# Optimization experiments

Hardware: AMD Instinct MI355X
Metric: run time of the kernel (lower is better)

## Reference

```python
import jax, jax.numpy as jnp
import numpy as np

NEG = -1e30  # log-space 'zero'


def setup_inputs() -> dict:
    N, T, IDIM, V, S = 16, 1024, 512, 4096, 128
    key = jax.random.key(0)
    k0, k1, k2, k3, k4 = jax.random.split(key, 5)
    hs = jax.random.normal(k0, (N, T, IDIM), dtype=jnp.float32)
    hlens = jax.random.randint(k1, (N,), T // 2, T + 1).astype(jnp.int32)
    ys = jax.random.randint(k2, (N, S), 1, V).astype(jnp.int32)  # labels exclude blank=0
    ylens = jax.random.randint(k3, (N,), S // 2, S + 1).astype(jnp.int32)
    W = jax.random.normal(k4, (V, IDIM), dtype=jnp.float32) * 0.02
    b = jnp.zeros((V,), dtype=jnp.float32)
    return {"hs": hs, "hlens": hlens, "ys": ys, "ylens": ylens, "W": W, "b": b}


def _ctc_loss(logp, hlens, ys, ylens):
    # logp: (N, T, V) log-softmax outputs; blank index = 0
    N, T, V = logp.shape
    S = ys.shape[1]
    L = 2 * S + 1
    # extended label sequence: blank, y1, blank, y2, ..., blank
    ext = jnp.zeros((N, L), dtype=ys.dtype).at[:, 1::2].set(ys)  # (N, L)
    s_idx = jnp.arange(L)
    ext_prev2 = jnp.pad(ext, ((0, 0), (2, 0)))[:, :L]
    allow_skip = (ext != 0) & (ext != ext_prev2) & (s_idx[None, :] >= 2)  # (N, L)
    Ln = 2 * ylens + 1  # valid extended length per sample

    lpT = jnp.swapaxes(logp, 0, 1)  # (T, N, V)

    # t = 0 init
    alpha0 = jnp.full((N, L), NEG, dtype=logp.dtype)
    alpha0 = alpha0.at[:, 0].set(lpT[0, :, 0])
    alpha0 = alpha0.at[:, 1].set(jnp.take_along_axis(lpT[0], ys[:, :1], axis=1)[:, 0])

    def step(alpha, xs):
        lp_t, t = xs  # lp_t: (N, V)
        lp_ext = jnp.take_along_axis(lp_t, ext, axis=1)  # (N, L)
        a1 = alpha
        a2 = jnp.pad(alpha, ((0, 0), (1, 0)), constant_values=NEG)[:, :L]
        a3 = jnp.pad(alpha, ((0, 0), (2, 0)), constant_values=NEG)[:, :L]
        a3 = jnp.where(allow_skip, a3, NEG)
        new = jnp.logaddexp(jnp.logaddexp(a1, a2), a3) + lp_ext
        new = jnp.where(s_idx[None, :] < Ln[:, None], new, NEG)
        alpha = jnp.where((t < hlens)[:, None], new, alpha)
        return alpha, None

    ts = jnp.arange(1, T, dtype=hlens.dtype)
    alpha, _ = jax.lax.scan(step, alpha0, (lpT[1:], ts))

    end1 = jnp.take_along_axis(alpha, (Ln - 1)[:, None], axis=1)[:, 0]
    end2 = jnp.take_along_axis(alpha, (Ln - 2)[:, None], axis=1)[:, 0]
    ll = jnp.logaddexp(end1, end2)  # (N,)
    per = jnp.where(ll > -1e29, -ll, 0.0)  # zero_infinity=True
    return jnp.sum(per) / N  # reduction='sum' then divided by len(hlens)


def reference(hs, hlens, ys, ylens, W, b):
    logits = jnp.einsum('nti,vi->ntv', hs, W) + b  # (N, T, V)
    logp = jax.nn.log_softmax(logits, axis=-1)
    return _ctc_loss(logp, hlens, ys, ylens)
```

## Files before the change

kernel.cpp:

```cpp
#include <hip/hip_runtime.h>
#include <cstdint>
#include <cstddef>

using short8_t = __attribute__((ext_vector_type(8))) short;
using f32x4    = __attribute__((ext_vector_type(4))) float;
typedef unsigned short bfu16;

constexpr int   Nn   = 16;
constexpr int   Tt   = 1024;
constexpr int   IDIM = 512;
constexpr int   Vv   = 4096;
constexpr int   Ss   = 128;
constexpr int   Ll   = 2 * Ss + 1;
constexpr int   LS   = 132;
constexpr float NEGV = -1e30f;
constexpr float L2E  = 1.4426950408889634f;
constexpr float LN2  = 0.6931471805599453f;

__device__ __forceinline__ float fexp2(float x) { return __builtin_amdgcn_exp2f(x); }
__device__ __forceinline__ float flog2(float x) { return __builtin_amdgcn_logf(x); }

__device__ __forceinline__ bfu16 f2bf(float f) {
  unsigned int x = __float_as_uint(f);
  x = x + 0x7fffu + ((x >> 16) & 1u);
  return (bfu16)(x >> 16);
}

__device__ __forceinline__ void async16(const void* g, void* l) {
  __builtin_amdgcn_global_load_lds(
      (__attribute__((address_space(1))) void*)(g),
      (__attribute__((address_space(3))) void*)(l), 16, 0, 0);
}

__global__ void convert_zero(const float4* __restrict__ hs4,
                             const float4* __restrict__ W4,
                             ushort4* __restrict__ hsb4,
                             ushort4* __restrict__ Wb4,
                             float* __restrict__ out) {
  if (blockIdx.x == 0 && threadIdx.x == 0) out[0] = 0.f;
  const int HS4 = (Nn * Tt * IDIM) / 4;
  const int TOT = HS4 + (Vv * IDIM) / 4;
  for (int i = blockIdx.x * 256 + threadIdx.x; i < TOT; i += gridDim.x * 256) {
    float4 f;
    if (i < HS4) f = hs4[i]; else f = W4[i - HS4];
    ushort4 o;
    o.x = f2bf(f.x); o.y = f2bf(f.y); o.z = f2bf(f.z); o.w = f2bf(f.w);
    if (i < HS4) hsb4[i] = o; else Wb4[i - HS4] = o;
  }
}

__global__ void build_labels(const int* __restrict__ ys,
                             int* __restrict__ labmap,
                             int* __restrict__ extidx,
                             int* __restrict__ skipflag) {
  const int n = blockIdx.x, tid = threadIdx.x;
  int* lm = labmap + n * Vv;
  for (int v = tid; v < Vv; v += 256) lm[v] = 0x7fffffff;
  __syncthreads();
  if (tid == 0) lm[0] = 0;
  if (tid < Ss) atomicMin(&lm[ys[n * Ss + tid]], tid + 1);
  __syncthreads();
  for (int s = tid; s < Ll; s += 256) {
    int v = (s & 1) ? ys[n * Ss + ((s - 1) >> 1)] : 0;
    extidx[n * Ll + s] = lm[v];
    int allow = 0;
    if ((s & 1) && s >= 3) allow = (v != ys[n * Ss + ((s - 3) >> 1)]) ? 1 : 0;
    skipflag[n * Ll + s] = allow;
  }
  __syncthreads();
  for (int v = tid; v < Vv; v += 256)
    if (lm[v] == 0x7fffffff) lm[v] = -1;
}

__global__ __launch_bounds__(512, 2) void gemm_lse(
    const bfu16* __restrict__ A,
    const bfu16* __restrict__ B,
    const float* __restrict__ bias,
    const int*   __restrict__ labmap,
    float* __restrict__ plab,
    float* __restrict__ psum) {
  __shared__ alignas(128) char ldsraw[131072];
  const int tid  = threadIdx.x;
  const int lane = tid & 63, wid = tid >> 6;
  const int wr = wid >> 2, wc = wid & 3;

  const int flat = blockIdx.x;
  const int wg   = (flat & 7) * 128 + (flat >> 3);
  const int bR = wg >> 4, bC = wg & 15;
  const int rowbase = bR * 256, colbase = bC * 256;

  f32x4 acc[8][4];
#pragma unroll
  for (int m = 0; m < 8; m++)
#pragma unroll
    for (int n = 0; n < 4; n++) {
      f32x4 z = {0.f, 0.f, 0.f, 0.f};
      acc[m][n] = z;
    }

  const int  sw  = wid & 3;
  const bool isB = wid >= 4;
  const char* gsrc0 = (const char*)(isB ? (const void*)B : (const void*)A)
      + (size_t)((isB ? colbase : rowbase) + sw * 64 + (lane >> 3)) * (IDIM * 2)
      + (((lane & 7) ^ ((lane >> 3) & 7)) * 16);
  char* ldst0 = ldsraw + (isB ? 32768 : 0) + sw * 8192;

  const int fr = lane & 15;
  const int g  = lane >> 4;
  const int fx = fr & 7;

  const int nsamp = bR >> 2;
  const int* lm = labmap + nsamp * Vv;
  float bc[4];
  int   slot[4];
#pragma unroll
  for (int n = 0; n < 4; n++) {
    int c = colbase + wc * 64 + n * 16 + fr;
    bc[n]   = bias[c];
    slot[n] = lm[c];
  }

  auto stage = [&](int b, int t) {
#pragma unroll
    for (int i = 0; i < 8; ++i)
      async16(gsrc0 + (size_t)t * 128 + i * 8192, ldst0 + b * 65536 + i * 1024);
  };

  stage(0, 0);
  asm volatile("s_waitcnt vmcnt(0)" ::: "memory");
  __builtin_amdgcn_s_barrier();

  int buf = 0;
  for (int t = 0; t < 8; ++t) {
    const char* Ab = ldsraw + buf * 65536;
    const char* Bb = Ab + 32768;
    if (t < 7) stage(buf ^ 1, t + 1);

    short8_t a0[4], a1[4], a2[4], a3[4], b0[4], b1[4];
#pragma unroll
    for (int m = 0; m < 4; m++)
      a0[m] = *(const short8_t*)(Ab + (wr * 128 + m * 16 + fr) * 128 + ((0 + g) ^ fx) * 16);
#pragma unroll
    for (int n = 0; n < 4; n++)
      b0[n] = *(const short8_t*)(Bb + (wc * 64 + n * 16 + fr) * 128 + ((0 + g) ^ fx) * 16);
#pragma unroll
    for (int m = 0; m < 4; m++)
      a1[m] = *(const short8_t*)(Ab + (wr * 128 + (m + 4) * 16 + fr) * 128 + ((0 + g) ^ fx) * 16);

    __builtin_amdgcn_s_setprio(1);
#pragma unroll
    for (int m = 0; m < 4; m++)
#pragma unroll
      for (int n = 0; n < 4; n++)
        acc[m][n] = __builtin_amdgcn_mfma_f32_16x16x32_bf16(a0[m], b0[n], acc[m][n], 0, 0, 0);
    __builtin_amdgcn_s_setprio(0);

#pragma unroll
    for (int m = 0; m < 4; m++)
      a2[m] = *(const short8_t*)(Ab + (wr * 128 + m * 16 + fr) * 128 + ((4 + g) ^ fx) * 16);
#pragma unroll
    for (int n = 0; n < 4; n++)
      b1[n] = *(const short8_t*)(Bb + (wc * 64 + n * 16 + fr) * 128 + ((4 + g) ^ fx) * 16);

    __builtin_amdgcn_s_setprio(1);
#pragma unroll
    for (int m = 0; m < 4; m++)
#pragma unroll
      for (int n = 0; n < 4; n++)
        acc[m + 4][n] = __builtin_amdgcn_mfma_f32_16x16x32_bf16(a1[m], b0[n], acc[m + 4][n], 0, 0, 0);
    __builtin_amdgcn_s_setprio(0);

#pragma unroll
    for (int m = 0; m < 4; m++)
      a3[m] = *(const short8_t*)(Ab + (wr * 128 + (m + 4) * 16 + fr) * 128 + ((4 + g) ^ fx) * 16);

    __builtin_amdgcn_s_setprio(1);
#pragma unroll
    for (int m = 0; m < 4; m++)
#pragma unroll
      for (int n = 0; n < 4; n++)
        acc[m][n] = __builtin_amdgcn_mfma_f32_16x16x32_bf16(a2[m], b1[n], acc[m][n], 0, 0, 0);
    __builtin_amdgcn_s_setprio(0);

    __builtin_amdgcn_s_setprio(1);
#pragma unroll
    for (int m = 0; m < 4; m++)
#pragma unroll
      for (int n = 0; n < 4; n++)
        acc[m + 4][n] = __builtin_amdgcn_mfma_f32_16x16x32_bf16(a3[m], b1[n], acc[m + 4][n], 0, 0, 0);
    __builtin_amdgcn_s_setprio(0);

    asm volatile("s_waitcnt vmcnt(0)" ::: "memory");
    __builtin_amdgcn_s_barrier();
    buf ^= 1;
  }

  const int g4 = g * 4;
#pragma unroll
  for (int m = 0; m < 8; m++) {
#pragma unroll
    for (int r = 0; r < 4; r++) {
      int row = rowbase + wr * 128 + m * 16 + g4 + r;
      float e0 = fexp2((acc[m][0][r] + bc[0]) * L2E);
      float e1 = fexp2((acc[m][1][r] + bc[1]) * L2E);
      float e2 = fexp2((acc[m][2][r] + bc[2]) * L2E);
      float e3 = fexp2((acc[m][3][r] + bc[3]) * L2E);
      if (slot[0] >= 0) plab[(size_t)row * LS + slot[0]] = e0;
      if (slot[1] >= 0) plab[(size_t)row * LS + slot[1]] = e1;
      if (slot[2] >= 0) plab[(size_t)row * LS + slot[2]] = e2;
      if (slot[3] >= 0) plab[(size_t)row * LS + slot[3]] = e3;
      float s = (e0 + e1) + (e2 + e3);
      s += __shfl_xor(s, 1);
      s += __shfl_xor(s, 2);
      s += __shfl_xor(s, 4);
      s += __shfl_xor(s, 8);
      if (fr == 0) {
        int pc = bC * 4 + wc;
        psum[(size_t)pc * 16384 + row] = s;
      }
    }
  }
}

__global__ void lse_reduce(const float* __restrict__ psum,
                           float* __restrict__ lse) {
  int row = blockIdx.x * 256 + threadIdx.x;
  float s = 0.f;
#pragma unroll 8
  for (int j = 0; j < 64; j++)
    s += psum[(size_t)j * 16384 + row];
  lse[row] = flog2(s) * LN2;
}

constexpr int BRK = 16;

__global__ __launch_bounds__(64) void ctc_dp(
    const float* __restrict__ plab, const float* __restrict__ lse,
    const int* __restrict__ extidx, const int* __restrict__ skipflag,
    const int* __restrict__ hlens, const int* __restrict__ ylens,
    float* __restrict__ out) {
  __shared__ float lbuf[2][2304];
  __shared__ float alf[264];
  const int n    = blockIdx.x;
  const int lane = threadIdx.x;
  const int hlen = hlens[n];
  const int Ln   = 2 * ylens[n] + 1;
  const int sbase = lane * 4;

  const int   e1  = extidx[n * Ll + sbase + 1];
  const int   e3  = extidx[n * Ll + sbase + 3];
  const float sk1 = skipflag[n * Ll + sbase + 1] ? 1.f : 0.f;
  const float sk3 = skipflag[n * Ll + sbase + 3] ? 1.f : 0.f;
  const float skh = (lane > 0 && skipflag[n * Ll + sbase - 1]) ? 1.f : 0.f;
  const float skz = (lane > 0 && skipflag[n * Ll + sbase - 3]) ? 1.f : 0.f;
  const float skv = (lane > 1 && skipflag[n * Ll + sbase - 5]) ? 1.f : 0.f;
  const bool  l0  = (lane == 0);
  const bool  l01 = (lane < 2);
  const float m0  = (sbase + 0 < Ln) ? 1.f : 0.f;
  const float m1  = (sbase + 1 < Ln) ? 1.f : 0.f;
  const float m2  = (sbase + 2 < Ln) ? 1.f : 0.f;
  const float m3  = (sbase + 3 < Ln) ? 1.f : 0.f;
  const float m4  = (lane == 63 && Ln == 257) ? 1.f : 0.f;

  const float* pl  = plab + (size_t)n * Tt * LS;
  const float* lsp = lse + n * Tt;

  float slse = 0.f;
#pragma unroll
  for (int j = 0; j < 16; j++) {
    int t = lane + 64 * j;
    float v = lsp[t];
    slse += (t < hlen) ? v : 0.f;
  }
#pragma unroll
  for (int off = 32; off; off >>= 1) slse += __shfl_xor(slse, off);

  float a0 = 0.f, a1 = 0.f, a2 = 0.f, a3 = 0.f, a4 = 0.f;
  if (l0) { a0 = pl[0]; a1 = pl[e1]; }

  int sc = 0;

  auto pair2 = [&](float pbA, float p1A, float p3A,
                   float pbB, float p1B, float p3B) {
    float pa3 = __shfl_up(a3, 1);
    float pa2 = __shfl_up(a2, 1);
    float pa1 = __shfl_up(a1, 1);
    float prA = __shfl_up(p3A, 1);
    pa3 = l0 ? 0.f : pa3;
    pa2 = l0 ? 0.f : pa2;
    pa1 = l0 ? 0.f : pa1;
    float h1 = (pa3 + pa2 + skh * pa1) * prA;
    float s4 = (a4 + a3) * pbA;
    float s3 = (a3 + a2 + sk3 * a1) * p3A;
    float s2 = (a2 + a1) * pbA;
    float s1 = (a1 + a0 + sk1 * pa3) * p1A;
    float s0 = (a0 + pa3) * pbA;
    a4 = (s4 + s3) * pbB;
    a3 = (s3 + s2 + sk3 * s1) * p3B;
    a2 = (s2 + s1) * pbB;
    a1 = (s1 + s0 + sk1 * h1) * p1B;
    a0 = (s0 + h1) * pbB;
  };

  auto step1 = [&](float pb, float p1, float p3) {
    float pm1 = __shfl_up(a3, 1);
    pm1 = l0 ? 0.f : pm1;
    float n4 = (a4 + a3) * pb;
    float n3 = (a3 + a2 + sk3 * a1) * p3;
    float n2 = (a2 + a1) * pb;
    float n1 = (a1 + a0 + sk1 * pm1) * p1;
    float n0 = (a0 + pm1) * pb;
    a0 = n0; a1 = n1; a2 = n2; a3 = n3; a4 = n4;
  };

  auto rescale = [&]() {
    a0 *= m0; a1 *= m1; a2 *= m2; a3 *= m3; a4 *= m4;
    float mx = fmaxf(fmaxf(a0, a1), fmaxf(a2, a3));
    mx = fmaxf(mx, a4);
#pragma unroll
    for (int off = 32; off; off >>= 1) mx = fmaxf(mx, __shfl_xor(mx, off));
    int ee = (int)((__float_as_uint(mx) >> 23) & 0xff) - 127;
    ee = (mx > 0.f) ? ee : 0;
    float s = __uint_as_float((unsigned)(127 - ee) << 23);
    sc += ee;
    a0 *= s; a1 *= s; a2 *= s; a3 *= s; a4 *= s;
  };

  auto stageblk = [&](int bsel, int row0) {
    const char* src = (const char*)(pl + (size_t)row0 * LS);
    char* dst = (char*)&lbuf[bsel][0];
#pragma unroll
    for (int i = 0; i < 9; ++i)
      async16(src + i * 1024 + lane * 16, dst + i * 1024);
  };

  float rpb[2][4], rp1[2][4], rp3[2][4];
  float rx3[2][3];
  float rz1[2][2];
  float rv3[2][1];

  auto loadring = [&](int slot, const float* Lb, int q) {
#pragma unroll
    for (int r = 0; r < 4; r++) {
      const float* base = Lb + (4 * q + r) * 132;
      rpb[slot][r] = base[0];
      rp1[slot][r] = base[e1];
      rp3[slot][r] = base[e3];
    }
#pragma unroll
    for (int r = 0; r < 3; r++) rx3[slot][r] = __shfl_up(rp3[slot][r], 1);
#pragma unroll
    for (int r = 0; r < 2; r++) rz1[slot][r] = __shfl_up(rp1[slot][r], 1);
    rv3[slot][0] = __shfl_up(rp3[slot][0], 2);
  };

  auto quad4 = [&](int slot) {
    float x0 = __shfl_up(a3, 1);
    float y0 = __shfl_up(a2, 1);
    float z0 = __shfl_up(a1, 1);
    float w0 = __shfl_up(a0, 1);
    float v0 = __shfl_up(a3, 2);
    float u0 = __shfl_up(a2, 2);
    float q0 = __shfl_up(a1, 2);
    x0 = l0 ? 0.f : x0;  y0 = l0 ? 0.f : y0;
    z0 = l0 ? 0.f : z0;  w0 = l0 ? 0.f : w0;
    v0 = l01 ? 0.f : v0; u0 = l01 ? 0.f : u0; q0 = l01 ? 0.f : q0;

    float v1 = (v0 + u0 + skv * q0) * rv3[slot][0];
    float w1 = (w0 + v0) * rpb[slot][0];
    float z1 = (z0 + w0 + skz * v0) * rz1[slot][0];
    float y1 = (y0 + z0) * rpb[slot][0];
    float x1 = (x0 + y0 + skh * z0) * rx3[slot][0];
    float z2 = (z1 + w1 + skz * v1) * rz1[slot][1];
    float y2 = (y1 + z1) * rpb[slot][1];
    float x2 = (x1 + y1 + skh * z1) * rx3[slot][1];
    float x3 = (x2 + y2 + skh * z2) * rx3[slot][2];

    float xk[4] = {x0, x1, x2, x3};
#pragma unroll
    for (int r = 0; r < 4; r++) {
      float pb = rpb[slot][r], p1 = rp1[slot][r], p3 = rp3[slot][r];
      float n4 = (a4 + a3) * pb;
      float n3 = (a3 + a2 + sk3 * a1) * p3;
      float n2 = (a2 + a1) * pb;
      float n1 = (a1 + a0 + sk1 * xk[r]) * p1;
      float n0 = (a0 + xk[r]) * pb;
      a0 = n0; a1 = n1; a2 = n2; a3 = n3; a4 = n4;
    }
  };

  const int nsteps = hlen - 1;
  const int nblk   = nsteps / BRK;

  if (nblk > 0) {
    stageblk(0, 1);
    asm volatile("s_waitcnt vmcnt(0)" ::: "memory");
  }

  for (int b = 0; b < nblk; b++) {
    if (b + 1 < nblk) stageblk((b + 1) & 1, 1 + BRK * (b + 1));
    const float* Lb = &lbuf[b & 1][0];
    loadring(0, Lb, 0);
#pragma unroll
    for (int q = 0; q < 4; q++) {
      if (q < 3) loadring((q + 1) & 1, Lb, q + 1);
      quad4(q & 1);
    }
    if ((b & 1) || b == nblk - 1) rescale();
    asm volatile("s_waitcnt vmcnt(0)" ::: "memory");
  }

  int t = 1 + nblk * BRK;
  for (; t + 1 <= nsteps; t += 2) {
    pair2(pl[(size_t)t * LS], pl[(size_t)t * LS + e1], pl[(size_t)t * LS + e3],
          pl[(size_t)(t + 1) * LS], pl[(size_t)(t + 1) * LS + e1], pl[(size_t)(t + 1) * LS + e3]);
  }
  if (t <= nsteps) {
    step1(pl[(size_t)t * LS], pl[(size_t)t * LS + e1], pl[(size_t)t * LS + e3]);
  }
  rescale();

  alf[sbase + 0] = a0; alf[sbase + 1] = a1;
  alf[sbase + 2] = a2; alf[sbase + 3] = a3;
  if (lane == 63) alf[256] = a4;
  __syncthreads();
  if (l0) {
    float sum = alf[Ln - 1] + alf[Ln - 2];
    float per = 0.f;
    if (sum > 0.f) {
      float llv = (flog2(sum) + (float)sc) * LN2 - slse;
      if (llv > -1e29f) per = -llv;
    }
    atomicAdd(out, per * (1.0f / 16.0f));
  }
}

extern "C" void kernel_launch(void* const* d_in, const int* in_sizes, int n_in,
                              void* d_out, int out_size, void* d_ws, size_t ws_size,
                              hipStream_t stream) {
  const float* hs    = (const float*)d_in[0];
  const int*   hlens = (const int*)d_in[1];
  const int*   ys    = (const int*)d_in[2];
  const int*   ylens = (const int*)d_in[3];
  const float* W     = (const float*)d_in[4];
  const float* bias  = (const float*)d_in[5];
  float*       out   = (float*)d_out;
  char*        ws    = (char*)d_ws;

  const size_t off_hsb    = 0;
  const size_t off_Wb     = off_hsb    + (size_t)Nn*Tt*IDIM*2;
  const size_t off_plab   = off_Wb     + (size_t)Vv*IDIM*2;
  const size_t off_psum   = off_plab   + (size_t)Nn*Tt*LS*4;
  const size_t off_lse    = off_psum   + (size_t)64*16384*4;
  const size_t off_labmap = off_lse    + (size_t)16384*4;
  const size_t off_extidx = off_labmap + (size_t)Nn*Vv*4;
  const size_t off_skip   = off_extidx + (size_t)((Nn*Ll*4 + 255) & ~255);

  bfu16* hsb    = (bfu16*)(ws + off_hsb);
  bfu16* Wb     = (bfu16*)(ws + off_Wb);
  float* plab   = (float*)(ws + off_plab);
  float* psum   = (float*)(ws + off_psum);
  float* lse    = (float*)(ws + off_lse);
  int*   labmap = (int*)(ws + off_labmap);
  int*   extidx = (int*)(ws + off_extidx);
  int*   skipf  = (int*)(ws + off_skip);

  convert_zero<<<2048, 256, 0, stream>>>(
      (const float4*)hs, (const float4*)W, (ushort4*)hsb, (ushort4*)Wb, out);
  build_labels<<<16, 256, 0, stream>>>(ys, labmap, extidx, skipf);
  gemm_lse<<<1024, 512, 0, stream>>>(hsb, Wb, bias, labmap, plab, psum);
  lse_reduce<<<64, 256, 0, stream>>>(psum, lse);
  ctc_dp<<<16, 64, 0, stream>>>(plab, lse, extidx, skipf, hlens, ylens, out);
}
```

Before: 209.4 us.

## Transpose label-probability buffer to slot-major and load DP inputs directly with float4

```diff
diff --git a/kernel.cpp b/kernel.cpp
--- a/kernel.cpp
+++ b/kernel.cpp
@@ -13,6 +13,7 @@
 constexpr int   Ss   = 128;
 constexpr int   Ll   = 2 * Ss + 1;
 constexpr int   LS   = 132;
+constexpr int   PST  = LS * Tt;
 constexpr float NEGV = -1e30f;
 constexpr float L2E  = 1.4426950408889634f;
 constexpr float LN2  = 0.6931471805599453f;
@@ -77,7 +78,7 @@
     const bfu16* __restrict__ B,
     const float* __restrict__ bias,
     const int*   __restrict__ labmap,
-    float* __restrict__ plab,
+    float* __restrict__ plabT,
     float* __restrict__ psum) {
   __shared__ alignas(128) char ldsraw[131072];
   const int tid  = threadIdx.x;
@@ -111,6 +112,7 @@
 
   const int nsamp = bR >> 2;
   const int* lm = labmap + nsamp * Vv;
+  float* plT = plabT + (size_t)nsamp * PST;
   float bc[4];
   int   slot[4];
 #pragma unroll
@@ -201,14 +203,15 @@
 #pragma unroll
     for (int r = 0; r < 4; r++) {
       int row = rowbase + wr * 128 + m * 16 + g4 + r;
+      int tIn = row & 1023;
       float e0 = fexp2((acc[m][0][r] + bc[0]) * L2E);
       float e1 = fexp2((acc[m][1][r] + bc[1]) * L2E);
       float e2 = fexp2((acc[m][2][r] + bc[2]) * L2E);
       float e3 = fexp2((acc[m][3][r] + bc[3]) * L2E);
-      if (slot[0] >= 0) plab[(size_t)row * LS + slot[0]] = e0;
-      if (slot[1] >= 0) plab[(size_t)row * LS + slot[1]] = e1;
-      if (slot[2] >= 0) plab[(size_t)row * LS + slot[2]] = e2;
-      if (slot[3] >= 0) plab[(size_t)row * LS + slot[3]] = e3;
+      if (slot[0] >= 0) plT[(size_t)slot[0] * Tt + tIn] = e0;
+      if (slot[1] >= 0) plT[(size_t)slot[1] * Tt + tIn] = e1;
+      if (slot[2] >= 0) plT[(size_t)slot[2] * Tt + tIn] = e2;
+      if (slot[3] >= 0) plT[(size_t)slot[3] * Tt + tIn] = e3;
       float s = (e0 + e1) + (e2 + e3);
       s += __shfl_xor(s, 1);
       s += __shfl_xor(s, 2);
@@ -232,14 +235,11 @@
   lse[row] = flog2(s) * LN2;
 }
 
-constexpr int BRK = 16;
-
 __global__ __launch_bounds__(64) void ctc_dp(
-    const float* __restrict__ plab, const float* __restrict__ lse,
+    const float* __restrict__ plabT, const float* __restrict__ lse,
     const int* __restrict__ extidx, const int* __restrict__ skipflag,
     const int* __restrict__ hlens, const int* __restrict__ ylens,
     float* __restrict__ out) {
-  __shared__ float lbuf[2][2304];
   __shared__ float alf[264];
   const int n    = blockIdx.x;
   const int lane = threadIdx.x;
@@ -262,7 +262,10 @@
   const float m3  = (sbase + 3 < Ln) ? 1.f : 0.f;
   const float m4  = (lane == 63 && Ln == 257) ? 1.f : 0.f;
 
-  const float* pl  = plab + (size_t)n * Tt * LS;
+  const float* pl  = plabT + (size_t)n * PST;
+  const float* rb  = pl;
+  const float* r1p = pl + (size_t)e1 * Tt;
+  const float* r3p = pl + (size_t)e3 * Tt;
   const float* lsp = lse + n * Tt;
 
   float slse = 0.f;
@@ -276,9 +279,20 @@
   for (int off = 32; off; off >>= 1) slse += __shfl_xor(slse, off);
 
   float a0 = 0.f, a1 = 0.f, a2 = 0.f, a3 = 0.f, a4 = 0.f;
-  if (l0) { a0 = pl[0]; a1 = pl[e1]; }
+  if (l0) { a0 = rb[0]; a1 = r1p[0]; }
 
   int sc = 0;
+
+  auto step1 = [&](float pb, float p1, float p3) {
+    float pm1 = __shfl_up(a3, 1);
+    pm1 = l0 ? 0.f : pm1;
+    float n4 = (a4 + a3) * pb;
+    float n3 = (a3 + a2 + sk3 * a1) * p3;
+    float n2 = (a2 + a1) * pb;
+    float n1 = (a1 + a0 + sk1 * pm1) * p1;
+    float n0 = (a0 + pm1) * pb;
+    a0 = n0; a1 = n1; a2 = n2; a3 = n3; a4 = n4;
+  };
 
   auto pair2 = [&](float pbA, float p1A, float p3A,
                    float pbB, float p1B, float p3B) {
@@ -302,17 +316,6 @@
     a0 = (s0 + h1) * pbB;
   };
 
-  auto step1 = [&](float pb, float p1, float p3) {
-    float pm1 = __shfl_up(a3, 1);
-    pm1 = l0 ? 0.f : pm1;
-    float n4 = (a4 + a3) * pb;
-    float n3 = (a3 + a2 + sk3 * a1) * p3;
-    float n2 = (a2 + a1) * pb;
-    float n1 = (a1 + a0 + sk1 * pm1) * p1;
-    float n0 = (a0 + pm1) * pb;
-    a0 = n0; a1 = n1; a2 = n2; a3 = n3; a4 = n4;
-  };
-
   auto rescale = [&]() {
     a0 *= m0; a1 *= m1; a2 *= m2; a3 *= m3; a4 *= m4;
     float mx = fmaxf(fmaxf(a0, a1), fmaxf(a2, a3));
@@ -326,97 +329,104 @@
     a0 *= s; a1 *= s; a2 *= s; a3 *= s; a4 *= s;
   };
 
-  auto stageblk = [&](int bsel, int row0) {
-    const char* src = (const char*)(pl + (size_t)row0 * LS);
-    char* dst = (char*)&lbuf[bsel][0];
-#pragma unroll
-    for (int i = 0; i < 9; ++i)
-      async16(src + i * 1024 + lane * 16, dst + i * 1024);
-  };
-
-  float rpb[2][4], rp1[2][4], rp3[2][4];
-  float rx3[2][3];
-  float rz1[2][2];
-  float rv3[2][1];
-
-  auto loadring = [&](int slot, const float* Lb, int q) {
-#pragma unroll
-    for (int r = 0; r < 4; r++) {
-      const float* base = Lb + (4 * q + r) * 132;
-      rpb[slot][r] = base[0];
-      rp1[slot][r] = base[e1];
-      rp3[slot][r] = base[e3];
-    }
-#pragma unroll
-    for (int r = 0; r < 3; r++) rx3[slot][r] = __shfl_up(rp3[slot][r], 1);
-#pragma unroll
-    for (int r = 0; r < 2; r++) rz1[slot][r] = __shfl_up(rp1[slot][r], 1);
-    rv3[slot][0] = __shfl_up(rp3[slot][0], 2);
-  };
-
-  auto quad4 = [&](int slot) {
-    float x0 = __shfl_up(a3, 1);
-    float y0 = __shfl_up(a2, 1);
-    float z0 = __shfl_up(a1, 1);
-    float w0 = __shfl_up(a0, 1);
-    float v0 = __shfl_up(a3, 2);
-    float u0 = __shfl_up(a2, 2);
-    float q0 = __shfl_up(a1, 2);
-    x0 = l0 ? 0.f : x0;  y0 = l0 ? 0.f : y0;
-    z0 = l0 ? 0.f : z0;  w0 = l0 ? 0.f : w0;
-    v0 = l01 ? 0.f : v0; u0 = l01 ? 0.f : u0; q0 = l01 ? 0.f : q0;
-
-    float v1 = (v0 + u0 + skv * q0) * rv3[slot][0];
-    float w1 = (w0 + v0) * rpb[slot][0];
-    float z1 = (z0 + w0 + skz * v0) * rz1[slot][0];
-    float y1 = (y0 + z0) * rpb[slot][0];
-    float x1 = (x0 + y0 + skh * z0) * rx3[slot][0];
-    float z2 = (z1 + w1 + skz * v1) * rz1[slot][1];
-    float y2 = (y1 + z1) * rpb[slot][1];
-    float x2 = (x1 + y1 + skh * z1) * rx3[slot][1];
-    float x3 = (x2 + y2 + skh * z2) * rx3[slot][2];
-
-    float xk[4] = {x0, x1, x2, x3};
-#pragma unroll
-    for (int r = 0; r < 4; r++) {
-      float pb = rpb[slot][r], p1 = rp1[slot][r], p3 = rp3[slot][r];
-      float n4 = (a4 + a3) * pb;
-      float n3 = (a3 + a2 + sk3 * a1) * p3;
-      float n2 = (a2 + a1) * pb;
-      float n1 = (a1 + a0 + sk1 * xk[r]) * p1;
-      float n0 = (a0 + xk[r]) * pb;
-      a0 = n0; a1 = n1; a2 = n2; a3 = n3; a4 = n4;
+  float pb_[2][4][4], p1_[2][4][4], p3_[2][4][4];
+  float hx_[2][4][3], hz_[2][4][2], hv_[2][4];
+
+  auto loadSB = [&](int sl, int t4) {
+#pragma unroll
+    for (int q = 0; q < 4; q++) {
+      float4 vb = *(const float4*)(rb  + t4 + 4 * q);
+      float4 v1 = *(const float4*)(r1p + t4 + 4 * q);
+      float4 v3 = *(const float4*)(r3p + t4 + 4 * q);
+      pb_[sl][q][0] = vb.x; pb_[sl][q][1] = vb.y; pb_[sl][q][2] = vb.z; pb_[sl][q][3] = vb.w;
+      p1_[sl][q][0] = v1.x; p1_[sl][q][1] = v1.y; p1_[sl][q][2] = v1.z; p1_[sl][q][3] = v1.w;
+      p3_[sl][q][0] = v3.x; p3_[sl][q][1] = v3.y; p3_[sl][q][2] = v3.z; p3_[sl][q][3] = v3.w;
+    }
+  };
+
+  auto haloSB = [&](int sl) {
+#pragma unroll
+    for (int q = 0; q < 4; q++) {
+      hx_[sl][q][0] = __shfl_up(p3_[sl][q][0], 1);
+      hx_[sl][q][1] = __shfl_up(p3_[sl][q][1], 1);
+      hx_[sl][q][2] = __shfl_up(p3_[sl][q][2], 1);
+      hz_[sl][q][0] = __shfl_up(p1_[sl][q][0], 1);
+      hz_[sl][q][1] = __shfl_up(p1_[sl][q][1], 1);
+      hv_[sl][q]    = __shfl_up(p3_[sl][q][0], 2);
+    }
+  };
+
+  auto quadsSB = [&](int sl) {
+#pragma unroll
+    for (int q = 0; q < 4; q++) {
+      float x0 = __shfl_up(a3, 1);
+      float y0 = __shfl_up(a2, 1);
+      float z0 = __shfl_up(a1, 1);
+      float w0 = __shfl_up(a0, 1);
+      float v0 = __shfl_up(a3, 2);
+      float u0 = __shfl_up(a2, 2);
+      float q0 = __shfl_up(a1, 2);
+      x0 = l0 ? 0.f : x0;  y0 = l0 ? 0.f : y0;
+      z0 = l0 ? 0.f : z0;  w0 = l0 ? 0.f : w0;
+      v0 = l01 ? 0.f : v0; u0 = l01 ? 0.f : u0; q0 = l01 ? 0.f : q0;
+
+      float v1 = (v0 + u0 + skv * q0) * hv_[sl][q];
+      float w1 = (w0 + v0) * pb_[sl][q][0];
+      float z1 = (z0 + w0 + skz * v0) * hz_[sl][q][0];
+      float y1 = (y0 + z0) * pb_[sl][q][0];
+      float x1 = (x0 + y0 + skh * z0) * hx_[sl][q][0];
+      float z2 = (z1 + w1 + skz * v1) * hz_[sl][q][1];
+      float y2 = (y1 + z1) * pb_[sl][q][1];
+      float x2 = (x1 + y1 + skh * z1) * hx_[sl][q][1];
+      float x3 = (x2 + y2 + skh * z2) * hx_[sl][q][2];
+
+      float xk[4] = {x0, x1, x2, x3};
+#pragma unroll
+      for (int r = 0; r < 4; r++) {
+        float pb = pb_[sl][q][r], p1v = p1_[sl][q][r], p3v = p3_[sl][q][r];
+        float n4 = (a4 + a3) * pb;
+        float n3 = (a3 + a2 + sk3 * a1) * p3v;
+        float n2 = (a2 + a1) * pb;
+        float n1 = (a1 + a0 + sk1 * xk[r]) * p1v;
+        float n0 = (a0 + xk[r]) * pb;
+        a0 = n0; a1 = n1; a2 = n2; a3 = n3; a4 = n4;
+      }
     }
   };
 
   const int nsteps = hlen - 1;
-  const int nblk   = nsteps / BRK;
-
-  if (nblk > 0) {
-    stageblk(0, 1);
-    asm volatile("s_waitcnt vmcnt(0)" ::: "memory");
-  }
-
-  for (int b = 0; b < nblk; b++) {
-    if (b + 1 < nblk) stageblk((b + 1) & 1, 1 + BRK * (b + 1));
-    const float* Lb = &lbuf[b & 1][0];
-    loadring(0, Lb, 0);
-#pragma unroll
-    for (int q = 0; q < 4; q++) {
-      if (q < 3) loadring((q + 1) & 1, Lb, q + 1);
-      quad4(q & 1);
-    }
-    if ((b & 1) || b == nblk - 1) rescale();
-    asm volatile("s_waitcnt vmcnt(0)" ::: "memory");
-  }
-
-  int t = 1 + nblk * BRK;
+
+  int t = 1;
+  while (t < 4 && t <= nsteps) {
+    step1(rb[t], r1p[t], r3p[t]);
+    ++t;
+  }
+
+  const int nSB = (nsteps >= 19) ? (nsteps - 3) / 16 : 0;
+  int t4 = 4;
+  if (nSB > 0) loadSB(0, t4);
+
+  int done = 0;
+  while (done + 2 <= nSB) {
+    if (done + 1 < nSB) loadSB(1, t4 + 16);
+    haloSB(0); quadsSB(0);
+    if (done + 2 < nSB) loadSB(0, t4 + 32);
+    haloSB(1); quadsSB(1);
+    rescale();
+    done += 2; t4 += 32;
+  }
+  if (done < nSB) {
+    haloSB(0); quadsSB(0);
+    rescale();
+    t4 += 16;
+  }
+  t = 4 + 16 * nSB;
+
   for (; t + 1 <= nsteps; t += 2) {
-    pair2(pl[(size_t)t * LS], pl[(size_t)t * LS + e1], pl[(size_t)t * LS + e3],
-          pl[(size_t)(t + 1) * LS], pl[(size_t)(t + 1) * LS + e1], pl[(size_t)(t + 1) * LS + e3]);
+    pair2(rb[t], r1p[t], r3p[t], rb[t + 1], r1p[t + 1], r3p[t + 1]);
   }
   if (t <= nsteps) {
-    step1(pl[(size_t)t * LS], pl[(size_t)t * LS + e1], pl[(size_t)t * LS + e3]);
+    step1(rb[t], r1p[t], r3p[t]);
   }
   rescale();
 
@@ -450,7 +460,7 @@
   const size_t off_hsb    = 0;
   const size_t off_Wb     = off_hsb    + (size_t)Nn*Tt*IDIM*2;
   const size_t off_plab   = off_Wb     + (size_t)Vv*IDIM*2;
-  const size_t off_psum   = off_plab   + (size_t)Nn*Tt*LS*4;
+  const size_t off_psum   = off_plab   + (size_t)Nn*LS*Tt*4;
   const size_t off_lse    = off_psum   + (size_t)64*16384*4;
   const size_t off_labmap = off_lse    + (size_t)16384*4;
   const size_t off_extidx = off_labmap + (size_t)Nn*Vv*4;
@@ -458,7 +468,7 @@
 
   bfu16* hsb    = (bfu16*)(ws + off_hsb);
   bfu16* Wb     = (bfu16*)(ws + off_Wb);
-  float* plab   = (float*)(ws + off_plab);
+  float* plabT  = (float*)(ws + off_plab);
   float* psum   = (float*)(ws + off_psum);
   float* lse    = (float*)(ws + off_lse);
   int*   labmap = (int*)(ws + off_labmap);
@@ -468,7 +478,7 @@
   convert_zero<<<2048, 256, 0, stream>>>(
       (const float4*)hs, (const float4*)W, (ushort4*)hsb, (ushort4*)Wb, out);
   build_labels<<<16, 256, 0, stream>>>(ys, labmap, extidx, skipf);
-  gemm_lse<<<1024, 512, 0, stream>>>(hsb, Wb, bias, labmap, plab, psum);
+  gemm_lse<<<1024, 512, 0, stream>>>(hsb, Wb, bias, labmap, plabT, psum);
   lse_reduce<<<64, 256, 0, stream>>>(psum, lse);
-  ctc_dp<<<16, 64, 0, stream>>>(plab, lse, extidx, skipf, hlens, ylens, out);
-}
+  ctc_dp<<<16, 64, 0, stream>>>(plabT, lse, extidx, skipf, hlens, ylens, out);
+}
```

After: 200.9 us. 1.04x faster.
